# Kernel optimization log

Measured on AMD Instinct MI355X. Metric: run time of the kernel, lower is better.

Reference implementation:

```python
import jax, jax.numpy as jnp
import numpy as np

LST = 64  # sparsemax frame length over time


def sparsemax(z):
    """Sparsemax over the last axis (Martins & Astudillo 2016)."""
    d = z.shape[-1]
    z_sorted = jnp.flip(jnp.sort(z, axis=-1), axis=-1)           # descending
    z_cumsum = jnp.cumsum(z_sorted, axis=-1)
    k = jnp.arange(1, d + 1, dtype=z.dtype)
    support = (1.0 + k * z_sorted) > z_cumsum                    # bool, [..., d]
    k_z = jnp.sum(support, axis=-1, keepdims=True)               # int, >=1
    tau_sum = jnp.take_along_axis(z_cumsum, k_z - 1, axis=-1)
    tau = (tau_sum - 1.0) / k_z.astype(z.dtype)
    return jnp.maximum(z - tau, 0.0)


def setup_inputs() -> dict:
    key = jax.random.key(0)
    midis_out = jax.random.normal(key, (16, 11, 65536), dtype=jnp.float32)
    return {"midis_out": midis_out}


def reference(midis_out):
    batch, n_insts, time = midis_out.shape
    lst = LST
    len_pad = (lst - time % lst) % lst
    x = jnp.pad(midis_out, ((0, 0), (0, 0), (0, len_pad)))
    t_pad = time + len_pad
    # sparsemax over instruments: (b, t, i) -> sparsemax over i -> back to (b, i, t)
    out_inst = jnp.swapaxes(sparsemax(jnp.swapaxes(x, 1, 2)), 1, 2)
    # sparsemax over fixed time blocks of length lst
    out_time = sparsemax(x.reshape(batch, n_insts, t_pad // lst, lst))
    out_time = out_time.reshape(batch, n_insts, t_pad)
    return out_inst[:, :, :time] * out_time[:, :, :time]
```

## Files before the change

### kernel.cpp

```cpp
#include <hip/hip_runtime.h>

#define B_   16
#define NI   11
#define T_   65536
#define LST  64
#define NBLK (T_ / LST)
#define ROWP 68

__device__ __forceinline__ float frcp(float x) { return __builtin_amdgcn_rcpf(x); }

__global__ __launch_bounds__(256) void fused_sparsemax_kernel(
        const float* __restrict__ in, float* __restrict__ out) {
    __shared__ float ldsz[4][NI * ROWP];
    __shared__ float ldsti[4][64];

    const int lane = threadIdx.x & 63;
    const int wid  = threadIdx.x >> 6;
    const int tile = blockIdx.x * 4 + wid;
    const int b    = tile >> 10;
    const int jb   = tile & (NBLK - 1);

    const float* px = in + (size_t)b * NI * T_ + (size_t)jb * LST + (size_t)lane;

    float z[NI];
#pragma unroll
    for (int i = 0; i < NI; ++i) z[i] = px[(size_t)i * T_];

#pragma unroll
    for (int i = 0; i < NI; ++i) ldsz[wid][i * ROWP + lane] = z[i];

    float mx = z[0];
#pragma unroll
    for (int i = 1; i < NI; ++i) mx = fmaxf(mx, z[i]);
    float tau_i = mx - 1.0f;
    float prevc = 0.0f;
    for (int it = 0; it < NI + 2; ++it) {
        float sp = 0.0f, cp = 0.0f;
#pragma unroll
        for (int i = 0; i < NI; ++i) {
            bool a = z[i] > tau_i;
            sp += a ? z[i] : 0.0f;
            cp += a ? 1.0f : 0.0f;
        }
        bool changed = (cp != prevc);
        if (!__any(changed)) break;
        prevc = cp;
        tau_i = (sp - 1.0f) * frcp(cp);
    }
    ldsti[wid][lane] = tau_i;

    const int g   = lane >> 2;
    const int q   = lane & 3;
    const int row = (g < NI) ? g : (g - NI);

    float y[16];
#pragma unroll
    for (int r = 0; r < 16; ++r) y[r] = ldsz[wid][row * ROWP + q * 16 + r];

    float m = y[0];
#pragma unroll
    for (int r = 1; r < 16; ++r) m = fmaxf(m, y[r]);
    m = fmaxf(m, __shfl_xor(m, 1, 64));
    m = fmaxf(m, __shfl_xor(m, 2, 64));
    float tau = m - 1.0f;
    float prev = 0.0f;
    for (int it = 0; it < LST + 2; ++it) {
        float sp = 0.0f, cp = 0.0f;
#pragma unroll
        for (int r = 0; r < 16; ++r) {
            bool a = y[r] > tau;
            sp += a ? y[r] : 0.0f;
            cp += a ? 1.0f : 0.0f;
        }
        sp += __shfl_xor(sp, 1, 64);
        sp += __shfl_xor(sp, 2, 64);
        cp += __shfl_xor(cp, 1, 64);
        cp += __shfl_xor(cp, 2, 64);
        bool changed = (cp != prev);
        if (!__any(changed)) break;
        prev = cp;
        tau = (sp - 1.0f) * frcp(cp);
    }

    if (g < NI) {
        float ti[16];
#pragma unroll
        for (int r = 0; r < 16; ++r) ti[r] = ldsti[wid][q * 16 + r];

        float* po = out + (size_t)b * NI * T_ + (size_t)g * T_
                        + (size_t)jb * LST + (size_t)q * 16;
        float4* po4 = reinterpret_cast<float4*>(po);
#pragma unroll
        for (int v = 0; v < 4; ++v) {
            float4 o;
            o.x = fmaxf(y[4*v+0] - tau, 0.0f) * fmaxf(y[4*v+0] - ti[4*v+0], 0.0f);
            o.y = fmaxf(y[4*v+1] - tau, 0.0f) * fmaxf(y[4*v+1] - ti[4*v+1], 0.0f);
            o.z = fmaxf(y[4*v+2] - tau, 0.0f) * fmaxf(y[4*v+2] - ti[4*v+2], 0.0f);
            o.w = fmaxf(y[4*v+3] - tau, 0.0f) * fmaxf(y[4*v+3] - ti[4*v+3], 0.0f);
            po4[v] = o;
        }
    }
}

extern "C" void kernel_launch(void* const* d_in, const int* in_sizes, int n_in,
                              void* d_out, int out_size, void* d_ws, size_t ws_size,
                              hipStream_t stream) {
    const float* in = (const float*)d_in[0];
    float* out = (float*)d_out;
    hipLaunchKernelGGL(fused_sparsemax_kernel, dim3(4096), dim3(256), 0, stream,
                       in, out);
}
```

Baseline: 27.57 us.

## Process two time blocks per wave with float2 loads and DPP reductions

Each wavefront now handles 128 time steps (two sparsemax frames) instead of 64. Each lane loads float2 per instrument, and the grid is halved accordingly. Cross-lane reductions within groups of four lanes use DPP quad permutes instead of __shfl_xor, which avoids the LDS-based permute path. This also raises the occupancy hint via launch_bounds, at the cost of more registers per thread and more serialized work per wave.

```diff
diff --git a/kernel.cpp b/kernel.cpp
--- a/kernel.cpp
+++ b/kernel.cpp
@@ -4,100 +4,123 @@
 #define NI   11
 #define T_   65536
 #define LST  64
-#define NBLK (T_ / LST)
-#define ROWP 68
+#define ROW2 132
+
+#define DPP_XOR1 0xB1
+#define DPP_XOR2 0x4E
 
 __device__ __forceinline__ float frcp(float x) { return __builtin_amdgcn_rcpf(x); }
 
-__global__ __launch_bounds__(256) void fused_sparsemax_kernel(
+template<int CTRL>
+__device__ __forceinline__ float dppf(float x) {
+    return __int_as_float(__builtin_amdgcn_update_dpp(
+        0, __float_as_int(x), CTRL, 0xF, 0xF, true));
+}
+
+__global__ __launch_bounds__(256, 6) void fused_sparsemax_kernel(
         const float* __restrict__ in, float* __restrict__ out) {
-    __shared__ float ldsz[4][NI * ROWP];
-    __shared__ float ldsti[4][64];
+    __shared__ float ldsz[4][NI * ROW2];
+    __shared__ float ldsti[4][128];
 
     const int lane = threadIdx.x & 63;
     const int wid  = threadIdx.x >> 6;
-    const int tile = blockIdx.x * 4 + wid;
-    const int b    = tile >> 10;
-    const int jb   = tile & (NBLK - 1);
+    const int st   = blockIdx.x * 4 + wid;
+    const int b    = st >> 9;
+    const int j2   = st & 511;
 
-    const float* px = in + (size_t)b * NI * T_ + (size_t)jb * LST + (size_t)lane;
+    const float* px = in + (size_t)b * NI * T_ + (size_t)j2 * 128
+                         + (size_t)lane * 2;
 
-    float z[NI];
+    float2 z[NI];
 #pragma unroll
-    for (int i = 0; i < NI; ++i) z[i] = px[(size_t)i * T_];
+    for (int i = 0; i < NI; ++i)
+        z[i] = *reinterpret_cast<const float2*>(px + (size_t)i * T_);
 
 #pragma unroll
-    for (int i = 0; i < NI; ++i) ldsz[wid][i * ROWP + lane] = z[i];
+    for (int i = 0; i < NI; ++i)
+        *reinterpret_cast<float2*>(&ldsz[wid][i * ROW2 + lane * 2]) = z[i];
 
-    float mx = z[0];
+    float mxa = z[0].x, mxb = z[0].y;
 #pragma unroll
-    for (int i = 1; i < NI; ++i) mx = fmaxf(mx, z[i]);
-    float tau_i = mx - 1.0f;
-    float prevc = 0.0f;
+    for (int i = 1; i < NI; ++i) {
+        mxa = fmaxf(mxa, z[i].x);
+        mxb = fmaxf(mxb, z[i].y);
+    }
+    float ta = mxa - 1.0f, tb = mxb - 1.0f;
+    float pa = 0.0f, pb = 0.0f;
     for (int it = 0; it < NI + 2; ++it) {
-        float sp = 0.0f, cp = 0.0f;
+        float sa = 0.0f, ca = 0.0f, sb = 0.0f, cb = 0.0f;
 #pragma unroll
         for (int i = 0; i < NI; ++i) {
-            bool a = z[i] > tau_i;
-            sp += a ? z[i] : 0.0f;
-            cp += a ? 1.0f : 0.0f;
+            bool aa = z[i].x > ta;
+            sa += aa ? z[i].x : 0.0f;
+            ca += aa ? 1.0f : 0.0f;
+            bool ab = z[i].y > tb;
+            sb += ab ? z[i].y : 0.0f;
+            cb += ab ? 1.0f : 0.0f;
         }
-        bool changed = (cp != prevc);
+        bool changed = (ca != pa) || (cb != pb);
         if (!__any(changed)) break;
-        prevc = cp;
-        tau_i = (sp - 1.0f) * frcp(cp);
+        pa = ca; pb = cb;
+        ta = (sa - 1.0f) * frcp(ca);
+        tb = (sb - 1.0f) * frcp(cb);
     }
-    ldsti[wid][lane] = tau_i;
+    *reinterpret_cast<float2*>(&ldsti[wid][lane * 2]) = make_float2(ta, tb);
 
     const int g   = lane >> 2;
     const int q   = lane & 3;
     const int row = (g < NI) ? g : (g - NI);
 
-    float y[16];
 #pragma unroll
-    for (int r = 0; r < 16; ++r) y[r] = ldsz[wid][row * ROWP + q * 16 + r];
+    for (int tile = 0; tile < 2; ++tile) {
+        const int cb = tile * 64 + q * 16;
 
-    float m = y[0];
+        float y[16];
 #pragma unroll
-    for (int r = 1; r < 16; ++r) m = fmaxf(m, y[r]);
-    m = fmaxf(m, __shfl_xor(m, 1, 64));
-    m = fmaxf(m, __shfl_xor(m, 2, 64));
-    float tau = m - 1.0f;
-    float prev = 0.0f;
-    for (int it = 0; it < LST + 2; ++it) {
-        float sp = 0.0f, cp = 0.0f;
+        for (int r = 0; r < 16; ++r) y[r] = ldsz[wid][row * ROW2 + cb + r];
+
+        float m = y[0];
 #pragma unroll
-        for (int r = 0; r < 16; ++r) {
-            bool a = y[r] > tau;
-            sp += a ? y[r] : 0.0f;
-            cp += a ? 1.0f : 0.0f;
+        for (int r = 1; r < 16; ++r) m = fmaxf(m, y[r]);
+        m = fmaxf(m, dppf<DPP_XOR1>(m));
+        m = fmaxf(m, dppf<DPP_XOR2>(m));
+
+        float tau = m - 1.0f, prev = 0.0f;
+        for (int it = 0; it < LST + 2; ++it) {
+            float sp = 0.0f, cp = 0.0f;
+#pragma unroll
+            for (int r = 0; r < 16; ++r) {
+                bool a = y[r] > tau;
+                sp += a ? y[r] : 0.0f;
+                cp += a ? 1.0f : 0.0f;
+            }
+            sp += dppf<DPP_XOR1>(sp);
+            sp += dppf<DPP_XOR2>(sp);
+            cp += dppf<DPP_XOR1>(cp);
+            cp += dppf<DPP_XOR2>(cp);
+            bool changed = (cp != prev);
+            if (!__any(changed)) break;
+            prev = cp;
+            tau = (sp - 1.0f) * frcp(cp);
         }
-        sp += __shfl_xor(sp, 1, 64);
-        sp += __shfl_xor(sp, 2, 64);
-        cp += __shfl_xor(cp, 1, 64);
-        cp += __shfl_xor(cp, 2, 64);
-        bool changed = (cp != prev);
-        if (!__any(changed)) break;
-        prev = cp;
-        tau = (sp - 1.0f) * frcp(cp);
-    }
 
-    if (g < NI) {
-        float ti[16];
+        if (g < NI) {
+            float ti[16];
 #pragma unroll
-        for (int r = 0; r < 16; ++r) ti[r] = ldsti[wid][q * 16 + r];
+            for (int r = 0; r < 16; ++r) ti[r] = ldsti[wid][cb + r];
 
-        float* po = out + (size_t)b * NI * T_ + (size_t)g * T_
-                        + (size_t)jb * LST + (size_t)q * 16;
-        float4* po4 = reinterpret_cast<float4*>(po);
+            float* po = out + (size_t)b * NI * T_ + (size_t)g * T_
+                            + (size_t)j2 * 128 + cb;
+            float4* po4 = reinterpret_cast<float4*>(po);
 #pragma unroll
-        for (int v = 0; v < 4; ++v) {
-            float4 o;
-            o.x = fmaxf(y[4*v+0] - tau, 0.0f) * fmaxf(y[4*v+0] - ti[4*v+0], 0.0f);
-            o.y = fmaxf(y[4*v+1] - tau, 0.0f) * fmaxf(y[4*v+1] - ti[4*v+1], 0.0f);
-            o.z = fmaxf(y[4*v+2] - tau, 0.0f) * fmaxf(y[4*v+2] - ti[4*v+2], 0.0f);
-            o.w = fmaxf(y[4*v+3] - tau, 0.0f) * fmaxf(y[4*v+3] - ti[4*v+3], 0.0f);
-            po4[v] = o;
+            for (int v = 0; v < 4; ++v) {
+                float4 o;
+                o.x = fmaxf(y[4*v+0] - tau, 0.0f) * fmaxf(y[4*v+0] - ti[4*v+0], 0.0f);
+                o.y = fmaxf(y[4*v+1] - tau, 0.0f) * fmaxf(y[4*v+1] - ti[4*v+1], 0.0f);
+                o.z = fmaxf(y[4*v+2] - tau, 0.0f) * fmaxf(y[4*v+2] - ti[4*v+2], 0.0f);
+                o.w = fmaxf(y[4*v+3] - tau, 0.0f) * fmaxf(y[4*v+3] - ti[4*v+3], 0.0f);
+                po4[v] = o;
+            }
         }
     }
 }
@@ -107,6 +130,6 @@
                               hipStream_t stream) {
     const float* in = (const float*)d_in[0];
     float* out = (float*)d_out;
-    hipLaunchKernelGGL(fused_sparsemax_kernel, dim3(4096), dim3(256), 0, stream,
+    hipLaunchKernelGGL(fused_sparsemax_kernel, dim3(2048), dim3(256), 0, stream,
                        in, out);
 }
```

Result: slower. 29.15 us (+5.8%).
